# Kernel tuning notes

Measured on AMD Instinct MI355X. Metric: run time of the kernel, lower is better.

## Reference

```python
import jax, jax.numpy as jnp
import numpy as np

DIN = 128
HID = 128
B, N = 32, 2048
NEG = 9000000000000000.0


def setup_inputs() -> dict:
    key = jax.random.key(0)
    ks = jax.random.split(key, 8)
    x = jax.random.normal(ks[0], (B, N, DIN), dtype=jnp.float32)
    mask = jax.random.randint(ks[1], (B, N, N), 0, 2).astype(jnp.float32)
    s = 1.0 / np.sqrt(DIN)
    Wv = jax.random.uniform(ks[2], (DIN, HID), minval=-s, maxval=s, dtype=jnp.float32)
    bv = jax.random.uniform(ks[3], (HID,), minval=-s, maxval=s, dtype=jnp.float32)
    Wk = jax.random.uniform(ks[4], (DIN, HID), minval=-s, maxval=s, dtype=jnp.float32)
    bk = jax.random.uniform(ks[5], (HID,), minval=-s, maxval=s, dtype=jnp.float32)
    Wq = jax.random.uniform(ks[6], (DIN, HID), minval=-s, maxval=s, dtype=jnp.float32)
    bq = jax.random.uniform(ks[7], (HID,), minval=-s, maxval=s, dtype=jnp.float32)
    return {"x": x, "mask": mask, "Wv": Wv, "bv": bv, "Wk": Wk, "bk": bk, "Wq": Wq, "bq": bq}


def reference(x, mask, Wv, bv, Wk, bk, Wq, bq):
    v = jnp.tanh(x @ Wv + bv)            # [B, N, H]
    q = jnp.tanh(x @ Wq + bq)            # [B, N, H]
    k = jnp.tanh(x @ Wk + bk)            # [B, N, H]
    scores = jnp.einsum('bih,bjh->bij', q, k)  # [B, N, N]
    scores = scores * mask - NEG * (1.0 - mask)
    att = jax.nn.softmax(scores, axis=-1)
    out = jnp.einsum('bij,bjh->bih', att, v)   # [B, N, H]
    return out
```

## Files before the change

kernel.cpp:

```cpp
#include <hip/hip_runtime.h>

#define DIN 128
#define HID 128
#define BB  32
#define NN  2048

typedef float  f32x4  __attribute__((ext_vector_type(4)));
typedef __bf16 bf16x8 __attribute__((ext_vector_type(8)));

__device__ __forceinline__ float tanh_fast(float x) {
  float e = __expf(2.0f * x);
  return 1.0f - 2.0f / (e + 1.0f);
}

__global__ __launch_bounds__(256) void wt_kernel(
    const float* __restrict__ Wq, const float* __restrict__ Wk,
    const float* __restrict__ Wv, __bf16* __restrict__ wt) {
  const float* W = (blockIdx.x == 0) ? Wq : (blockIdx.x == 1) ? Wk : Wv;
  __bf16* dst = wt + blockIdx.x * (DIN * HID);
  int t = threadIdx.x;
#pragma unroll
  for (int c = 0; c < 16; ++c) {
    int o = c * 1024 + t * 4;
    int d = o >> 7, h = o & 127;
    f32x4 v = *(const f32x4*)(W + d * HID + h);
    dst[(h + 0) * DIN + d] = (__bf16)v.x;
    dst[(h + 1) * DIN + d] = (__bf16)v.y;
    dst[(h + 2) * DIN + d] = (__bf16)v.z;
    dst[(h + 3) * DIN + d] = (__bf16)v.w;
  }
}

__global__ __launch_bounds__(256) void proj_kernel(
    const float* __restrict__ x, const __bf16* __restrict__ wt,
    const float* __restrict__ bq, const float* __restrict__ bk,
    const float* __restrict__ bv, __bf16* __restrict__ qbf,
    __bf16* __restrict__ kbf, __bf16* __restrict__ vtbf) {
  int tid = threadIdx.x;
  int lane = tid & 63, w = tid >> 6;
  int l15 = lane & 15, quad = lane >> 4;
  long i0 = (long)blockIdx.x * 64;

  bf16x8 bx[4][4];
#pragma unroll
  for (int nt = 0; nt < 4; ++nt) {
    const float* xp = x + (i0 + nt * 16 + l15) * DIN;
#pragma unroll
    for (int ks = 0; ks < 4; ++ks) {
      int d0 = ks * 32 + quad * 8;
      f32x4 a = *(const f32x4*)(xp + d0);
      f32x4 b = *(const f32x4*)(xp + d0 + 4);
      bf16x8 f;
      f[0] = (__bf16)a.x; f[1] = (__bf16)a.y; f[2] = (__bf16)a.z; f[3] = (__bf16)a.w;
      f[4] = (__bf16)b.x; f[5] = (__bf16)b.y; f[6] = (__bf16)b.z; f[7] = (__bf16)b.w;
      bx[nt][ks] = f;
    }
  }

#pragma unroll
  for (int p = 0; p < 2; ++p) {
    const __bf16* wtp = wt + p * DIN * HID;
    const float* bias = (p == 0) ? bq : bk;
    __bf16* outp = (p == 0) ? qbf : kbf;
#pragma unroll
    for (int nt = 0; nt < 8; ++nt) {
      int h0 = nt * 16 + l15;
      f32x4 acc = {0.f, 0.f, 0.f, 0.f};
#pragma unroll
      for (int ks = 0; ks < 4; ++ks) {
        bf16x8 wf = *(const bf16x8*)(wtp + (long)h0 * DIN + ks * 32 + quad * 8);
        acc = __builtin_amdgcn_mfma_f32_16x16x32_bf16(bx[w][ks], wf, acc, 0, 0, 0);
      }
      float bcol = bias[h0];
      long rowb = i0 + w * 16 + quad * 4;
#pragma unroll
      for (int r = 0; r < 4; ++r) {
        float val = tanh_fast(acc[r] + bcol);
        outp[(rowb + r) * HID + h0] = (__bf16)val;
      }
    }
  }

  {
    const __bf16* wtp = wt + 2 * DIN * HID;
    long bb = i0 >> 11;
    int nloc = (int)(i0 & 2047);
    long vbase = bb * (long)HID * NN;
#pragma unroll
    for (int s = 0; s < 2; ++s) {
      int hb = w * 32 + s * 16;
      bf16x8 af[4];
#pragma unroll
      for (int ks = 0; ks < 4; ++ks)
        af[ks] = *(const bf16x8*)(wtp + (long)(hb + l15) * DIN + ks * 32 + quad * 8);
      float bvr[4];
#pragma unroll
      for (int r = 0; r < 4; ++r) bvr[r] = bv[hb + quad * 4 + r];
#pragma unroll
      for (int nt = 0; nt < 4; ++nt) {
        f32x4 acc = {0.f, 0.f, 0.f, 0.f};
#pragma unroll
        for (int ks = 0; ks < 4; ++ks)
          acc = __builtin_amdgcn_mfma_f32_16x16x32_bf16(af[ks], bx[nt][ks], acc, 0, 0, 0);
        int hrow = hb + quad * 4;
        int ncol = nloc + nt * 16 + l15;
#pragma unroll
        for (int r = 0; r < 4; ++r) {
          float val = tanh_fast(acc[r] + bvr[r]);
          vtbf[vbase + (long)(hrow + r) * NN + ncol] = (__bf16)val;
        }
      }
    }
  }
}

#define KSTR 136
#define VSTR 72
#define PSTR 72

__global__ __launch_bounds__(256) void attn_kernel(
    const __bf16* __restrict__ qbf, const __bf16* __restrict__ kbf,
    const __bf16* __restrict__ vtbf, const float* __restrict__ mask,
    float* __restrict__ out) {
  __shared__ __bf16 Ks[64 * KSTR];
  __shared__ __bf16 Vts[128 * VSTR];
  __shared__ __bf16 Pl[4 * 16 * PSTR];

  int tid = threadIdx.x;
  int lane = tid & 63, w = tid >> 6;
  int l15 = lane & 15, quad = lane >> 4;
  int bid = blockIdx.x;
  int b = bid >> 5;
  int i0 = (bid & 31) * 64;
  long kvbase = (long)b * NN * HID;

  bf16x8 qf[4];
  {
    const __bf16* qp = qbf + kvbase + (long)(i0 + w * 16 + l15) * HID;
#pragma unroll
    for (int ks = 0; ks < 4; ++ks)
      qf[ks] = *(const bf16x8*)(qp + ks * 32 + quad * 8);
  }

  f32x4 O[8];
#pragma unroll
  for (int i = 0; i < 8; ++i) O[i] = (f32x4){0.f, 0.f, 0.f, 0.f};
  float mrow[4], lrow[4];
#pragma unroll
  for (int r = 0; r < 4; ++r) { mrow[r] = -1e30f; lrow[r] = 0.0f; }

  const float* maskrow =
      mask + ((long)b * NN + (i0 + w * 16 + quad * 4)) * NN;
  __bf16* Pw = Pl + w * 16 * PSTR;

  for (int jt = 0; jt < 32; ++jt) {
    int j0 = jt * 64;
    {
      const __bf16* ksrc = kbf + kvbase + (long)j0 * HID;
#pragma unroll
      for (int pass = 0; pass < 4; ++pass) {
        int o = pass * 2048 + tid * 8;
        int row = o >> 7, col = o & 127;
        bf16x8 v = *(const bf16x8*)(ksrc + (long)row * HID + col);
        *(bf16x8*)(Ks + row * KSTR + col) = v;
      }
      const __bf16* vsrc = vtbf + (long)b * HID * NN + j0;
#pragma unroll
      for (int pass = 0; pass < 4; ++pass) {
        int o = pass * 2048 + tid * 8;
        int h = o >> 6, c = o & 63;
        bf16x8 v = *(const bf16x8*)(vsrc + (long)h * NN + c);
        *(bf16x8*)(Vts + h * VSTR + c) = v;
      }
    }
    float mv[4][4];
#pragma unroll
    for (int t = 0; t < 4; ++t)
#pragma unroll
      for (int r = 0; r < 4; ++r)
        mv[t][r] = maskrow[(long)r * NN + j0 + t * 16 + l15];
    __syncthreads();

    f32x4 S[4];
#pragma unroll
    for (int t = 0; t < 4; ++t) {
      f32x4 acc = {0.f, 0.f, 0.f, 0.f};
      const __bf16* kp = Ks + (t * 16 + l15) * KSTR;
#pragma unroll
      for (int ks = 0; ks < 4; ++ks) {
        bf16x8 kf = *(const bf16x8*)(kp + ks * 32 + quad * 8);
        acc = __builtin_amdgcn_mfma_f32_16x16x32_bf16(qf[ks], kf, acc, 0, 0, 0);
      }
      S[t] = acc;
    }

    float p[4][4], alpha[4];
#pragma unroll
    for (int r = 0; r < 4; ++r) {
      float s0 = (mv[0][r] != 0.0f) ? S[0][r] : -1e30f;
      float s1 = (mv[1][r] != 0.0f) ? S[1][r] : -1e30f;
      float s2 = (mv[2][r] != 0.0f) ? S[2][r] : -1e30f;
      float s3 = (mv[3][r] != 0.0f) ? S[3][r] : -1e30f;
      float mx = fmaxf(fmaxf(s0, s1), fmaxf(s2, s3));
      mx = fmaxf(mx, __shfl_xor(mx, 1));
      mx = fmaxf(mx, __shfl_xor(mx, 2));
      mx = fmaxf(mx, __shfl_xor(mx, 4));
      mx = fmaxf(mx, __shfl_xor(mx, 8));
      float mnew = fmaxf(mrow[r], mx);
      alpha[r] = __expf(mrow[r] - mnew);
      float p0 = __expf(s0 - mnew), p1 = __expf(s1 - mnew);
      float p2 = __expf(s2 - mnew), p3 = __expf(s3 - mnew);
      p[0][r] = p0; p[1][r] = p1; p[2][r] = p2; p[3][r] = p3;
      float rs = p0 + p1 + p2 + p3;
      rs += __shfl_xor(rs, 1);
      rs += __shfl_xor(rs, 2);
      rs += __shfl_xor(rs, 4);
      rs += __shfl_xor(rs, 8);
      lrow[r] = lrow[r] * alpha[r] + rs;
      mrow[r] = mnew;
    }
#pragma unroll
    for (int nt = 0; nt < 8; ++nt)
#pragma unroll
      for (int r = 0; r < 4; ++r) O[nt][r] *= alpha[r];

#pragma unroll
    for (int t = 0; t < 4; ++t)
#pragma unroll
      for (int r = 0; r < 4; ++r)
        Pw[(quad * 4 + r) * PSTR + t * 16 + l15] = (__bf16)p[t][r];
    bf16x8 pf[2];
#pragma unroll
    for (int js = 0; js < 2; ++js)
      pf[js] = *(const bf16x8*)(Pw + l15 * PSTR + js * 32 + quad * 8);

#pragma unroll
    for (int nt = 0; nt < 8; ++nt) {
      const __bf16* vp = Vts + (nt * 16 + l15) * VSTR;
#pragma unroll
      for (int js = 0; js < 2; ++js) {
        bf16x8 vf = *(const bf16x8*)(vp + js * 32 + quad * 8);
        O[nt] = __builtin_amdgcn_mfma_f32_16x16x32_bf16(pf[js], vf, O[nt], 0, 0, 0);
      }
    }
    __syncthreads();
  }

  {
    long rowb = (long)b * NN + i0 + w * 16 + quad * 4;
#pragma unroll
    for (int r = 0; r < 4; ++r) {
      float inv = 1.0f / lrow[r];
      float* op = out + (rowb + r) * HID;
#pragma unroll
      for (int nt = 0; nt < 8; ++nt) op[nt * 16 + l15] = O[nt][r] * inv;
    }
  }
}

extern "C" void kernel_launch(void* const* d_in, const int* in_sizes, int n_in,
                              void* d_out, int out_size, void* d_ws, size_t ws_size,
                              hipStream_t stream) {
  const float* x    = (const float*)d_in[0];
  const float* mask = (const float*)d_in[1];
  const float* Wv   = (const float*)d_in[2];
  const float* bv   = (const float*)d_in[3];
  const float* Wk   = (const float*)d_in[4];
  const float* bk   = (const float*)d_in[5];
  const float* Wq   = (const float*)d_in[6];
  const float* bq   = (const float*)d_in[7];
  float* out = (float*)d_out;

  __bf16* ws = (__bf16*)d_ws;
  __bf16* wt   = ws;
  __bf16* qbf  = ws + 3 * DIN * HID;
  __bf16* kbf  = qbf + (long)BB * NN * HID;
  __bf16* vtbf = kbf + (long)BB * NN * HID;

  wt_kernel<<<3, 256, 0, stream>>>(Wq, Wk, Wv, wt);
  proj_kernel<<<BB * NN / 64, 256, 0, stream>>>(x, wt, bq, bk, bv, qbf, kbf, vtbf);
  attn_kernel<<<BB * (NN / 64), 256, 0, stream>>>(qbf, kbf, vtbf, mask, out);
}
```

Baseline: 1.052 ms.

## Restructure attention kernel with register prefetch, transposed scores and bigger blocks

The attention kernel now uses 512-thread blocks covering 128 query rows, with a remapped block index for K/V locality. The next K/V tile and mask values are prefetched into registers while the current tile computes. Scores are computed transposed so each lane owns one query row, which reduces softmax reductions to two shuffles. The mask is packed into a bitfield, float4 mask loads are used, and Q is prescaled by log2e so exp2f can replace expf. The extra live registers and the larger shared allocation may reduce occupancy.

After: 842.9 us. -19.9%, faster.

```diff
diff --git a/kernel.cpp b/kernel.cpp
--- a/kernel.cpp
+++ b/kernel.cpp
@@ -4,9 +4,11 @@
 #define HID 128
 #define BB  32
 #define NN  2048
-
-typedef float  f32x4  __attribute__((ext_vector_type(4)));
-typedef __bf16 bf16x8 __attribute__((ext_vector_type(8)));
+#define LOG2E 1.44269504088896340736f
+
+typedef float  f32x4   __attribute__((ext_vector_type(4)));
+typedef __bf16 bf16x4v __attribute__((ext_vector_type(4)));
+typedef __bf16 bf16x8  __attribute__((ext_vector_type(8)));
 
 __device__ __forceinline__ float tanh_fast(float x) {
   float e = __expf(2.0f * x);
@@ -76,6 +78,7 @@
 #pragma unroll
       for (int r = 0; r < 4; ++r) {
         float val = tanh_fast(acc[r] + bcol);
+        if (p == 0) val *= LOG2E;
         outp[(rowb + r) * HID + h0] = (__bf16)val;
       }
     }
@@ -118,143 +121,172 @@
 #define VSTR 72
 #define PSTR 72
 
-__global__ __launch_bounds__(256) void attn_kernel(
+__global__ __launch_bounds__(512, 4) void attn_kernel(
     const __bf16* __restrict__ qbf, const __bf16* __restrict__ kbf,
     const __bf16* __restrict__ vtbf, const float* __restrict__ mask,
     float* __restrict__ out) {
   __shared__ __bf16 Ks[64 * KSTR];
   __shared__ __bf16 Vts[128 * VSTR];
-  __shared__ __bf16 Pl[4 * 16 * PSTR];
-
-  int tid = threadIdx.x;
-  int lane = tid & 63, w = tid >> 6;
-  int l15 = lane & 15, quad = lane >> 4;
-  int bid = blockIdx.x;
-  int b = bid >> 5;
-  int i0 = (bid & 31) * 64;
-  long kvbase = (long)b * NN * HID;
+  __shared__ __bf16 Pl[8 * 16 * PSTR];
+
+  const int tid = threadIdx.x;
+  const int lane = tid & 63, w = tid >> 6;
+  const int l15 = lane & 15, quad = lane >> 4;
+  const int bid = blockIdx.x;
+  const int vb = (bid >> 3) | ((bid & 7) << 6);
+  const int b = vb >> 4;
+  const int i0 = (vb & 15) * 128;
+  const long kvbase = (long)b * NN * HID;
 
   bf16x8 qf[4];
   {
-    const __bf16* qp = qbf + kvbase + (long)(i0 + w * 16 + l15) * HID;
-#pragma unroll
-    for (int ks = 0; ks < 4; ++ks)
-      qf[ks] = *(const bf16x8*)(qp + ks * 32 + quad * 8);
-  }
+    const __bf16* qp = qbf + kvbase + (long)(i0 + w * 16 + l15) * HID + quad * 8;
+#pragma unroll
+    for (int ks = 0; ks < 4; ++ks) qf[ks] = *(const bf16x8*)(qp + ks * 32);
+  }
+
+  const int krow = tid >> 4, kcol = (tid & 15) * 8;
+  const int vrow = tid >> 3, vcol = (tid & 7) * 8;
+  const __bf16* kg = kbf + kvbase + (long)krow * HID + kcol;
+  const __bf16* vg = vtbf + (long)b * HID * NN + (long)vrow * NN + vcol;
+  __bf16* ksd0 = Ks + krow * KSTR + kcol;
+  __bf16* ksd1 = Ks + (krow + 32) * KSTR + kcol;
+  __bf16* vsd0 = Vts + vrow * VSTR + vcol;
+  __bf16* vsd1 = Vts + (vrow + 64) * VSTR + vcol;
+  const float* mp = mask + ((long)b * NN + (i0 + w * 16 + l15)) * NN + quad * 4;
+  __bf16* Pw = Pl + w * 16 * PSTR;
 
   f32x4 O[8];
 #pragma unroll
   for (int i = 0; i < 8; ++i) O[i] = (f32x4){0.f, 0.f, 0.f, 0.f};
-  float mrow[4], lrow[4];
-#pragma unroll
-  for (int r = 0; r < 4; ++r) { mrow[r] = -1e30f; lrow[r] = 0.0f; }
-
-  const float* maskrow =
-      mask + ((long)b * NN + (i0 + w * 16 + quad * 4)) * NN;
-  __bf16* Pw = Pl + w * 16 * PSTR;
+  float mrow = -1e30f, lrow = 0.0f;
+
+  bf16x8 kr0 = *(const bf16x8*)(kg);
+  bf16x8 kr1 = *(const bf16x8*)(kg + 32 * HID);
+  bf16x8 vr0 = *(const bf16x8*)(vg);
+  bf16x8 vr1 = *(const bf16x8*)(vg + (long)64 * NN);
+  f32x4 mr[4];
+#pragma unroll
+  for (int t = 0; t < 4; ++t) mr[t] = *(const f32x4*)(mp + t * 16);
+  *(bf16x8*)ksd0 = kr0; *(bf16x8*)ksd1 = kr1;
+  *(bf16x8*)vsd0 = vr0; *(bf16x8*)vsd1 = vr1;
+  unsigned mbits;
+  {
+    float mb = 0.f;
+#pragma unroll
+    for (int t = 0; t < 4; ++t)
+#pragma unroll
+      for (int r = 0; r < 4; ++r)
+        mb = fmaf(mr[t][r], (float)(1u << (t * 4 + r)), mb);
+    mbits = (unsigned)mb;
+  }
+  __syncthreads();
 
   for (int jt = 0; jt < 32; ++jt) {
-    int j0 = jt * 64;
+    const int jn = (jt < 31) ? jt + 1 : 31;
     {
-      const __bf16* ksrc = kbf + kvbase + (long)j0 * HID;
-#pragma unroll
-      for (int pass = 0; pass < 4; ++pass) {
-        int o = pass * 2048 + tid * 8;
-        int row = o >> 7, col = o & 127;
-        bf16x8 v = *(const bf16x8*)(ksrc + (long)row * HID + col);
-        *(bf16x8*)(Ks + row * KSTR + col) = v;
-      }
-      const __bf16* vsrc = vtbf + (long)b * HID * NN + j0;
-#pragma unroll
-      for (int pass = 0; pass < 4; ++pass) {
-        int o = pass * 2048 + tid * 8;
-        int h = o >> 6, c = o & 63;
-        bf16x8 v = *(const bf16x8*)(vsrc + (long)h * NN + c);
-        *(bf16x8*)(Vts + h * VSTR + c) = v;
-      }
-    }
-    float mv[4][4];
-#pragma unroll
-    for (int t = 0; t < 4; ++t)
-#pragma unroll
-      for (int r = 0; r < 4; ++r)
-        mv[t][r] = maskrow[(long)r * NN + j0 + t * 16 + l15];
-    __syncthreads();
-
-    f32x4 S[4];
+      const __bf16* kgn = kg + (long)jn * 64 * HID;
+      kr0 = *(const bf16x8*)(kgn);
+      kr1 = *(const bf16x8*)(kgn + 32 * HID);
+      const __bf16* vgn = vg + jn * 64;
+      vr0 = *(const bf16x8*)(vgn);
+      vr1 = *(const bf16x8*)(vgn + (long)64 * NN);
+#pragma unroll
+      for (int t = 0; t < 4; ++t) mr[t] = *(const f32x4*)(mp + jn * 64 + t * 16);
+    }
+
+    f32x4 pt[4];
 #pragma unroll
     for (int t = 0; t < 4; ++t) {
       f32x4 acc = {0.f, 0.f, 0.f, 0.f};
-      const __bf16* kp = Ks + (t * 16 + l15) * KSTR;
+      const __bf16* kp = Ks + (t * 16 + l15) * KSTR + quad * 8;
 #pragma unroll
       for (int ks = 0; ks < 4; ++ks) {
-        bf16x8 kf = *(const bf16x8*)(kp + ks * 32 + quad * 8);
-        acc = __builtin_amdgcn_mfma_f32_16x16x32_bf16(qf[ks], kf, acc, 0, 0, 0);
-      }
-      S[t] = acc;
-    }
-
-    float p[4][4], alpha[4];
-#pragma unroll
-    for (int r = 0; r < 4; ++r) {
-      float s0 = (mv[0][r] != 0.0f) ? S[0][r] : -1e30f;
-      float s1 = (mv[1][r] != 0.0f) ? S[1][r] : -1e30f;
-      float s2 = (mv[2][r] != 0.0f) ? S[2][r] : -1e30f;
-      float s3 = (mv[3][r] != 0.0f) ? S[3][r] : -1e30f;
-      float mx = fmaxf(fmaxf(s0, s1), fmaxf(s2, s3));
-      mx = fmaxf(mx, __shfl_xor(mx, 1));
-      mx = fmaxf(mx, __shfl_xor(mx, 2));
-      mx = fmaxf(mx, __shfl_xor(mx, 4));
-      mx = fmaxf(mx, __shfl_xor(mx, 8));
-      float mnew = fmaxf(mrow[r], mx);
-      alpha[r] = __expf(mrow[r] - mnew);
-      float p0 = __expf(s0 - mnew), p1 = __expf(s1 - mnew);
-      float p2 = __expf(s2 - mnew), p3 = __expf(s3 - mnew);
-      p[0][r] = p0; p[1][r] = p1; p[2][r] = p2; p[3][r] = p3;
-      float rs = p0 + p1 + p2 + p3;
-      rs += __shfl_xor(rs, 1);
-      rs += __shfl_xor(rs, 2);
-      rs += __shfl_xor(rs, 4);
-      rs += __shfl_xor(rs, 8);
-      lrow[r] = lrow[r] * alpha[r] + rs;
-      mrow[r] = mnew;
-    }
+        bf16x8 kf = *(const bf16x8*)(kp + ks * 32);
+        acc = __builtin_amdgcn_mfma_f32_16x16x32_bf16(kf, qf[ks], acc, 0, 0, 0);
+      }
+      pt[t] = acc;
+    }
+
+    float tmx = -1e30f;
+#pragma unroll
+    for (int t = 0; t < 4; ++t)
+#pragma unroll
+      for (int r = 0; r < 4; ++r) {
+        float s = ((mbits >> (t * 4 + r)) & 1u) ? pt[t][r] : -1e30f;
+        pt[t][r] = s;
+        tmx = fmaxf(tmx, s);
+      }
+    tmx = fmaxf(tmx, __shfl_xor(tmx, 16));
+    tmx = fmaxf(tmx, __shfl_xor(tmx, 32));
+    const float mnew = fmaxf(mrow, tmx);
+    const float alpha = exp2f(mrow - mnew);
+    float rs = 0.0f;
+#pragma unroll
+    for (int t = 0; t < 4; ++t)
+#pragma unroll
+      for (int r = 0; r < 4; ++r) {
+        float p = exp2f(pt[t][r] - mnew);
+        pt[t][r] = p;
+        rs += p;
+      }
+    rs += __shfl_xor(rs, 16);
+    rs += __shfl_xor(rs, 32);
+    lrow = lrow * alpha + rs;
+    mrow = mnew;
+
+    float ar[4];
+#pragma unroll
+    for (int r = 0; r < 4; ++r) ar[r] = __shfl(alpha, (quad << 2) + r);
 #pragma unroll
     for (int nt = 0; nt < 8; ++nt)
 #pragma unroll
-      for (int r = 0; r < 4; ++r) O[nt][r] *= alpha[r];
-
-#pragma unroll
-    for (int t = 0; t < 4; ++t)
-#pragma unroll
-      for (int r = 0; r < 4; ++r)
-        Pw[(quad * 4 + r) * PSTR + t * 16 + l15] = (__bf16)p[t][r];
-    bf16x8 pf[2];
-#pragma unroll
-    for (int js = 0; js < 2; ++js)
-      pf[js] = *(const bf16x8*)(Pw + l15 * PSTR + js * 32 + quad * 8);
+      for (int r = 0; r < 4; ++r) O[nt][r] *= ar[r];
+
+#pragma unroll
+    for (int t = 0; t < 4; ++t) {
+      bf16x4v pb;
+#pragma unroll
+      for (int r = 0; r < 4; ++r) pb[r] = (__bf16)pt[t][r];
+      *(bf16x4v*)(Pw + l15 * PSTR + t * 16 + quad * 4) = pb;
+    }
+    const bf16x8 pf0 = *(const bf16x8*)(Pw + l15 * PSTR + quad * 8);
+    const bf16x8 pf1 = *(const bf16x8*)(Pw + l15 * PSTR + 32 + quad * 8);
 
 #pragma unroll
     for (int nt = 0; nt < 8; ++nt) {
-      const __bf16* vp = Vts + (nt * 16 + l15) * VSTR;
-#pragma unroll
-      for (int js = 0; js < 2; ++js) {
-        bf16x8 vf = *(const bf16x8*)(vp + js * 32 + quad * 8);
-        O[nt] = __builtin_amdgcn_mfma_f32_16x16x32_bf16(pf[js], vf, O[nt], 0, 0, 0);
-      }
-    }
+      const __bf16* vp = Vts + (nt * 16 + l15) * VSTR + quad * 8;
+      bf16x8 vf0 = *(const bf16x8*)(vp);
+      bf16x8 vf1 = *(const bf16x8*)(vp + 32);
+      O[nt] = __builtin_amdgcn_mfma_f32_16x16x32_bf16(pf0, vf0, O[nt], 0, 0, 0);
+      O[nt] = __builtin_amdgcn_mfma_f32_16x16x32_bf16(pf1, vf1, O[nt], 0, 0, 0);
+    }
+
     __syncthreads();
-  }
-
-  {
-    long rowb = (long)b * NN + i0 + w * 16 + quad * 4;
-#pragma unroll
-    for (int r = 0; r < 4; ++r) {
-      float inv = 1.0f / lrow[r];
-      float* op = out + (rowb + r) * HID;
-#pragma unroll
-      for (int nt = 0; nt < 8; ++nt) op[nt * 16 + l15] = O[nt][r] * inv;
-    }
+    *(bf16x8*)ksd0 = kr0; *(bf16x8*)ksd1 = kr1;
+    *(bf16x8*)vsd0 = vr0; *(bf16x8*)vsd1 = vr1;
+    {
+      float mb = 0.f;
+#pragma unroll
+      for (int t = 0; t < 4; ++t)
+#pragma unroll
+        for (int r = 0; r < 4; ++r)
+          mb = fmaf(mr[t][r], (float)(1u << (t * 4 + r)), mb);
+      mbits = (unsigned)mb;
+    }
+    __syncthreads();
+  }
+
+  const float inv = 1.0f / lrow;
+  float il[4];
+#pragma unroll
+  for (int r = 0; r < 4; ++r) il[r] = __shfl(inv, (quad << 2) + r);
+  const long rowb = (long)b * NN + i0 + w * 16 + quad * 4;
+#pragma unroll
+  for (int r = 0; r < 4; ++r) {
+    float* op = out + (rowb + r) * HID;
+#pragma unroll
+    for (int nt = 0; nt < 8; ++nt) op[nt * 16 + l15] = O[nt][r] * il[r];
   }
 }
 
@@ -279,5 +311,5 @@
 
   wt_kernel<<<3, 256, 0, stream>>>(Wq, Wk, Wv, wt);
   proj_kernel<<<BB * NN / 64, 256, 0, stream>>>(x, wt, bq, bk, bv, qbf, kbf, vtbf);
-  attn_kernel<<<BB * (NN / 64), 256, 0, stream>>>(qbf, kbf, vtbf, mask, out);
-}
+  attn_kernel<<<512, 512, 0, stream>>>(qbf, kbf, vtbf, mask, out);
+}
```
